# Optimization experiments

Hardware: AMD Instinct MI355X
Metric: run time of the kernel (lower is better)

The kernel has to match this reference:

```python
import jax, jax.numpy as jnp
import numpy as np
import math

EPS = 1e-5      # artanh boundary clamp (Poincare ball)
MIN_NORM = 1e-15

def _norm(x):
    return jnp.clip(jnp.linalg.norm(x, axis=-1, keepdims=True), MIN_NORM, None)

def artanh(x):
    x = jnp.clip(x, -1.0 + EPS, 1.0 - EPS)
    return 0.5 * (jnp.log1p(x) - jnp.log1p(-x))

def expmap0(u):
    # c = 1 Poincare ball: tanh(||u||) * u / ||u||
    n = _norm(u)
    return jnp.tanh(n) * u / n

def mobius_matvec(M, x):
    # geoopt: mx = x @ M^T; res = tanh(||mx||/||x|| * artanh(||x||)) * mx/||mx||
    xn = _norm(x)
    mx = x @ M.T
    mxn = _norm(mx)
    res = jnp.tanh(mxn / xn * artanh(xn)) * mx / mxn
    zero_row = jnp.all(mx == 0, axis=-1, keepdims=True)
    return jnp.where(zero_row, jnp.zeros_like(res), res)

def mobius_add(x, y):
    x2 = jnp.sum(x * x, axis=-1, keepdims=True)
    y2 = jnp.sum(y * y, axis=-1, keepdims=True)
    xy = jnp.sum(x * y, axis=-1, keepdims=True)
    num = (1.0 + 2.0 * xy + y2) * x + (1.0 - x2) * y
    den = 1.0 + 2.0 * xy + x2 * y2
    return num / jnp.clip(den, MIN_NORM, None)

def dist(x, y):
    # d(x,y) = 2 * artanh(|| (-x) mobius+ y ||); reduces the last dim
    return 2.0 * artanh(_norm(mobius_add(-x, y)))[..., 0]

def setup_inputs() -> dict:
    key = jax.random.key(0)
    k1, k2, k3, k4, k5 = jax.random.split(key, 5)
    B, S, H, D = 64, 1024, 768, 64
    bound = 1.0 / math.sqrt(D)
    sequence_output = jax.random.normal(k1, (B, S, H), dtype=jnp.float32) * 0.1
    proj = jax.random.uniform(k2, (H, D), dtype=jnp.float32, minval=-0.05, maxval=0.05)
    trans = jax.random.uniform(k3, (D, D), dtype=jnp.float32, minval=-0.05, maxval=0.05)
    pos = expmap0(jax.random.uniform(k4, (D,), dtype=jnp.float32, minval=-bound, maxval=bound))
    neg = expmap0(jax.random.uniform(k5, (D,), dtype=jnp.float32, minval=-bound, maxval=bound))
    return {"sequence_output": sequence_output, "proj": proj, "trans": trans,
            "pos": pos, "neg": neg}

def reference(sequence_output, proj, trans, pos, neg):
    t = sequence_output @ proj          # [B, S, 64]
    t = expmap0(t)
    t = mobius_matvec(trans, t)
    pos_logits = dist(neg, t).sum(-1)   # [B]
    neg_logits = dist(pos, t).sum(-1)   # [B]
    return jnp.stack((neg_logits, pos_logits), axis=-1)  # [B, 2]
```

## Files before the change

### kernel.cpp

```cpp
#include <hip/hip_runtime.h>
#include <math.h>

#define MIN_NORM 1e-15f
#define BOUND_EPS 1e-5f

typedef __attribute__((ext_vector_type(8))) short short8v;
typedef __attribute__((ext_vector_type(4))) float f32x4;

__device__ __forceinline__ unsigned short f2bf(float f) {
  unsigned int u = __float_as_uint(f);
  unsigned int r = (u + 0x7FFFu + ((u >> 16) & 1u)) >> 16;
  return (unsigned short)r;
}

__device__ __forceinline__ float gred16(float v) {
  v += __shfl_xor(v, 1, 64);
  v += __shfl_xor(v, 2, 64);
  v += __shfl_xor(v, 4, 64);
  v += __shfl_xor(v, 8, 64);
  return v;
}
__device__ __forceinline__ float wred64(float v) {
#pragma unroll
  for (int off = 32; off; off >>= 1) v += __shfl_xor(v, off, 64);
  return v;
}
__device__ __forceinline__ float artanh_c(float x) {
  x = fminf(fmaxf(x, -1.f + BOUND_EPS), 1.f - BOUND_EPS);
  return 0.5f * logf((1.f + x) / (1.f - x));
}

__global__ __launch_bounds__(256) void poincare_prep(
    const float* __restrict__ proj, const float* __restrict__ trans,
    unsigned short* __restrict__ projB, unsigned short* __restrict__ transB) {
  int idx = blockIdx.x * 256 + threadIdx.x;
  if (idx < 49152) {
    int j = idx & 7, l = (idx >> 3) & 63, nt = (idx >> 9) & 3, kt = idx >> 11;
    projB[idx] = f2bf(proj[(kt * 32 + (l >> 4) * 8 + j) * 64 + nt * 16 + (l & 15)]);
  } else if (idx < 49152 + 4096) {
    int i2 = idx - 49152;
    int j = i2 & 7, l = (i2 >> 3) & 63, nt = (i2 >> 9) & 3, kt = i2 >> 11;
    transB[i2] = f2bf(trans[(nt * 16 + (l & 15)) * 64 + kt * 32 + (l >> 4) * 8 + j]);
  }
}

__global__ __launch_bounds__(256, 4) void poincare_main(
    const float* __restrict__ seq,
    const unsigned short* __restrict__ projB,
    const unsigned short* __restrict__ transB,
    const float* __restrict__ pos, const float* __restrict__ neg,
    float* __restrict__ wsPart) {
  __shared__ unsigned short teL[4][16 * 64];
  __shared__ float partial[4][2];

  const int tid = threadIdx.x;
  const int w = tid >> 6, l = tid & 63;
  const int lr = l & 15, lk = l >> 4;
  const long bIdx = blockIdx.x;

  const float* pA = seq + ((bIdx * 64 + w * 16 + lr) * 768 + lk * 8);
  const unsigned short* pB = projB + l * 8;

  f32x4 acc[4];
#pragma unroll
  for (int nt = 0; nt < 4; ++nt) acc[nt] = (f32x4){0.f, 0.f, 0.f, 0.f};

  for (int kt = 0; kt < 24; ++kt) {
    float4 a0 = *(const float4*)(pA);
    float4 a1 = *(const float4*)(pA + 4);
    pA += 32;
    const unsigned short* pb = pB + kt * 2048;
    short8v b0 = *(const short8v*)(pb);
    short8v b1 = *(const short8v*)(pb + 512);
    short8v b2 = *(const short8v*)(pb + 1024);
    short8v b3 = *(const short8v*)(pb + 1536);
    short8v av;
    av[0] = (short)f2bf(a0.x); av[1] = (short)f2bf(a0.y);
    av[2] = (short)f2bf(a0.z); av[3] = (short)f2bf(a0.w);
    av[4] = (short)f2bf(a1.x); av[5] = (short)f2bf(a1.y);
    av[6] = (short)f2bf(a1.z); av[7] = (short)f2bf(a1.w);
    acc[0] = __builtin_amdgcn_mfma_f32_16x16x32_bf16(av, b0, acc[0], 0, 0, 0);
    acc[1] = __builtin_amdgcn_mfma_f32_16x16x32_bf16(av, b1, acc[1], 0, 0, 0);
    acc[2] = __builtin_amdgcn_mfma_f32_16x16x32_bf16(av, b2, acc[2], 0, 0, 0);
    acc[3] = __builtin_amdgcn_mfma_f32_16x16x32_bf16(av, b3, acc[3], 0, 0, 0);
  }

  float th[4];
#pragma unroll
  for (int i = 0; i < 4; ++i) {
    float s = acc[0][i] * acc[0][i] + acc[1][i] * acc[1][i] +
              acc[2][i] * acc[2][i] + acc[3][i] * acc[3][i];
    s = gred16(s);
    float n = fmaxf(sqrtf(s), MIN_NORM);
    float t = tanhf(n);
    th[i] = fmaxf(t, MIN_NORM);
    float sc = t / n;
#pragma unroll
    for (int nt = 0; nt < 4; ++nt) acc[nt][i] *= sc;
  }

  unsigned short* buf = teL[w];
#pragma unroll
  for (int i = 0; i < 4; ++i) {
    int row = lk * 4 + i;
    int sw = (row & 7) << 3;
#pragma unroll
    for (int nt = 0; nt < 4; ++nt) {
      int col = nt * 16 + lr;
      buf[row * 64 + (col ^ sw)] = f2bf(acc[nt][i]);
    }
  }
  __syncthreads();

  f32x4 acc2[4];
#pragma unroll
  for (int nt = 0; nt < 4; ++nt) acc2[nt] = (f32x4){0.f, 0.f, 0.f, 0.f};
  const unsigned short* pT = transB + l * 8;
#pragma unroll
  for (int kt = 0; kt < 2; ++kt) {
    short8v a2 = *(const short8v*)&buf[lr * 64 + ((kt * 32 + lk * 8) ^ ((lr & 7) << 3))];
    const unsigned short* pt = pT + kt * 2048;
    short8v c0 = *(const short8v*)(pt);
    short8v c1 = *(const short8v*)(pt + 512);
    short8v c2 = *(const short8v*)(pt + 1024);
    short8v c3 = *(const short8v*)(pt + 1536);
    acc2[0] = __builtin_amdgcn_mfma_f32_16x16x32_bf16(a2, c0, acc2[0], 0, 0, 0);
    acc2[1] = __builtin_amdgcn_mfma_f32_16x16x32_bf16(a2, c1, acc2[1], 0, 0, 0);
    acc2[2] = __builtin_amdgcn_mfma_f32_16x16x32_bf16(a2, c2, acc2[2], 0, 0, 0);
    acc2[3] = __builtin_amdgcn_mfma_f32_16x16x32_bf16(a2, c3, acc2[3], 0, 0, 0);
  }

  float xp[4], xq[4];
#pragma unroll
  for (int nt = 0; nt < 4; ++nt) {
    xp[nt] = pos[nt * 16 + lr];
    xq[nt] = neg[nt * 16 + lr];
  }
  float x2p = wred64(xp[0] * xp[0] + xp[1] * xp[1] + xp[2] * xp[2] + xp[3] * xp[3]) * 0.25f;
  float x2n = wred64(xq[0] * xq[0] + xq[1] * xq[1] + xq[2] * xq[2] + xq[3] * xq[3]) * 0.25f;

  float distP = 0.f, distN = 0.f;
#pragma unroll
  for (int i = 0; i < 4; ++i) {
    float m0 = acc2[0][i], m1 = acc2[1][i], m2 = acc2[2][i], m3 = acc2[3][i];
    float s = gred16(m0 * m0 + m1 * m1 + m2 * m2 + m3 * m3);
    float mxn = fmaxf(sqrtf(s), MIN_NORM);
    float xn = th[i];
    float rs = tanhf(mxn / xn * artanh_c(xn)) / mxn;
    float r0 = rs * m0, r1 = rs * m1, r2 = rs * m2, r3 = rs * m3;
    float y2 = gred16(r0 * r0 + r1 * r1 + r2 * r2 + r3 * r3);
    float xyP = -gred16(xp[0] * r0 + xp[1] * r1 + xp[2] * r2 + xp[3] * r3);
    float xyN = -gred16(xq[0] * r0 + xq[1] * r1 + xq[2] * r2 + xq[3] * r3);
    {
      float A = 1.f + 2.f * xyP + y2, B = 1.f - x2p;
      float inv = 1.f / fmaxf(1.f + 2.f * xyP + x2p * y2, MIN_NORM);
      float v0 = (B * r0 - A * xp[0]) * inv, v1 = (B * r1 - A * xp[1]) * inv;
      float v2 = (B * r2 - A * xp[2]) * inv, v3 = (B * r3 - A * xp[3]) * inv;
      float nv = fmaxf(sqrtf(gred16(v0 * v0 + v1 * v1 + v2 * v2 + v3 * v3)), MIN_NORM);
      distP += 2.f * artanh_c(nv);
    }
    {
      float A = 1.f + 2.f * xyN + y2, B = 1.f - x2n;
      float inv = 1.f / fmaxf(1.f + 2.f * xyN + x2n * y2, MIN_NORM);
      float v0 = (B * r0 - A * xq[0]) * inv, v1 = (B * r1 - A * xq[1]) * inv;
      float v2 = (B * r2 - A * xq[2]) * inv, v3 = (B * r3 - A * xq[3]) * inv;
      float nv = fmaxf(sqrtf(gred16(v0 * v0 + v1 * v1 + v2 * v2 + v3 * v3)), MIN_NORM);
      distN += 2.f * artanh_c(nv);
    }
  }
  float tP = wred64(distP) * 0.0625f;
  float tN = wred64(distN) * 0.0625f;
  if (l == 0) { partial[w][0] = tP; partial[w][1] = tN; }
  __syncthreads();
  if (tid == 0)
    wsPart[bIdx * 2 + 0] = partial[0][0] + partial[1][0] + partial[2][0] + partial[3][0];
  if (tid == 1)
    wsPart[bIdx * 2 + 1] = partial[0][1] + partial[1][1] + partial[2][1] + partial[3][1];
}

__global__ __launch_bounds__(128) void poincare_reduce(const float* __restrict__ wsPart,
                                                       float* __restrict__ out) {
  int t = threadIdx.x;
  int b = t >> 1, j = t & 1;
  float s = 0.f;
#pragma unroll
  for (int i = 0; i < 16; ++i) s += wsPart[(b * 16 + i) * 2 + j];
  out[b * 2 + j] = s;
}

extern "C" void kernel_launch(void* const* d_in, const int* in_sizes, int n_in,
                              void* d_out, int out_size, void* d_ws, size_t ws_size,
                              hipStream_t stream) {
  const float* seq = (const float*)d_in[0];
  const float* proj = (const float*)d_in[1];
  const float* trans = (const float*)d_in[2];
  const float* pos = (const float*)d_in[3];
  const float* neg = (const float*)d_in[4];

  unsigned short* projB = (unsigned short*)d_ws;
  unsigned short* transB = projB + 49152;
  float* wsPart = (float*)((char*)d_ws + 106496);
  float* out = (float*)d_out;

  poincare_prep<<<208, 256, 0, stream>>>(proj, trans, projB, transB);
  poincare_main<<<1024, 256, 0, stream>>>(seq, projB, transB, pos, neg, wsPart);
  poincare_reduce<<<1, 128, 0, stream>>>(wsPart, out);
}
```

Before: 54.81 us.

## Split GEMM K dimension across two wave groups with LDS reduction

The main kernel now uses 512 threads per block. Two sets of four waves each compute half of the 768-wide K reduction for the same 64 rows, and the second half's partial accumulators are summed through a padded shared-memory buffer. The aim is to double the number of waves in flight, so the memory-bound streaming of the sequence input hides latency better. The cost is extra LDS traffic, two more barriers, and half the waves sitting idle during the epilogue.

```diff
diff --git a/kernel.cpp b/kernel.cpp
--- a/kernel.cpp
+++ b/kernel.cpp
@@ -44,28 +44,30 @@
   }
 }
 
-__global__ __launch_bounds__(256, 4) void poincare_main(
+__global__ __launch_bounds__(512, 8) void poincare_main(
     const float* __restrict__ seq,
     const unsigned short* __restrict__ projB,
     const unsigned short* __restrict__ transB,
     const float* __restrict__ pos, const float* __restrict__ neg,
     float* __restrict__ wsPart) {
   __shared__ unsigned short teL[4][16 * 64];
+  __shared__ float xbuf[4][64][17];
   __shared__ float partial[4][2];
 
   const int tid = threadIdx.x;
   const int w = tid >> 6, l = tid & 63;
+  const int p = w & 3, h = w >> 2;
   const int lr = l & 15, lk = l >> 4;
   const long bIdx = blockIdx.x;
 
-  const float* pA = seq + ((bIdx * 64 + w * 16 + lr) * 768 + lk * 8);
-  const unsigned short* pB = projB + l * 8;
+  const float* pA = seq + ((bIdx * 64 + p * 16 + lr) * 768 + h * 384 + lk * 8);
+  const unsigned short* pB = projB + h * 12 * 2048 + l * 8;
 
   f32x4 acc[4];
 #pragma unroll
   for (int nt = 0; nt < 4; ++nt) acc[nt] = (f32x4){0.f, 0.f, 0.f, 0.f};
 
-  for (int kt = 0; kt < 24; ++kt) {
+  for (int kt = 0; kt < 12; ++kt) {
     float4 a0 = *(const float4*)(pA);
     float4 a1 = *(const float4*)(pA + 4);
     pA += 32;
@@ -85,97 +87,115 @@
     acc[3] = __builtin_amdgcn_mfma_f32_16x16x32_bf16(av, b3, acc[3], 0, 0, 0);
   }
 
+  if (h) {
+#pragma unroll
+    for (int nt = 0; nt < 4; ++nt)
+#pragma unroll
+      for (int i = 0; i < 4; ++i) xbuf[p][l][nt * 4 + i] = acc[nt][i];
+  }
+  __syncthreads();
+
   float th[4];
-#pragma unroll
-  for (int i = 0; i < 4; ++i) {
-    float s = acc[0][i] * acc[0][i] + acc[1][i] * acc[1][i] +
-              acc[2][i] * acc[2][i] + acc[3][i] * acc[3][i];
-    s = gred16(s);
-    float n = fmaxf(sqrtf(s), MIN_NORM);
-    float t = tanhf(n);
-    th[i] = fmaxf(t, MIN_NORM);
-    float sc = t / n;
-#pragma unroll
-    for (int nt = 0; nt < 4; ++nt) acc[nt][i] *= sc;
-  }
-
-  unsigned short* buf = teL[w];
-#pragma unroll
-  for (int i = 0; i < 4; ++i) {
-    int row = lk * 4 + i;
-    int sw = (row & 7) << 3;
+  if (!h) {
+#pragma unroll
+    for (int nt = 0; nt < 4; ++nt)
+#pragma unroll
+      for (int i = 0; i < 4; ++i) acc[nt][i] += xbuf[p][l][nt * 4 + i];
+
+#pragma unroll
+    for (int i = 0; i < 4; ++i) {
+      float s = acc[0][i] * acc[0][i] + acc[1][i] * acc[1][i] +
+                acc[2][i] * acc[2][i] + acc[3][i] * acc[3][i];
+      s = gred16(s);
+      float n = fmaxf(sqrtf(s), MIN_NORM);
+      float t = tanhf(n);
+      th[i] = fmaxf(t, MIN_NORM);
+      float sc = t / n;
+#pragma unroll
+      for (int nt = 0; nt < 4; ++nt) acc[nt][i] *= sc;
+    }
+
+    unsigned short* buf = teL[p];
+#pragma unroll
+    for (int i = 0; i < 4; ++i) {
+      int row = lk * 4 + i;
+      int sw = (row & 7) << 3;
+#pragma unroll
+      for (int nt = 0; nt < 4; ++nt) {
+        int col = nt * 16 + lr;
+        buf[row * 64 + (col ^ sw)] = f2bf(acc[nt][i]);
+      }
+    }
+  }
+  __syncthreads();
+
+  if (!h) {
+    const unsigned short* buf = teL[p];
+    f32x4 acc2[4];
+#pragma unroll
+    for (int nt = 0; nt < 4; ++nt) acc2[nt] = (f32x4){0.f, 0.f, 0.f, 0.f};
+    const unsigned short* pT = transB + l * 8;
+#pragma unroll
+    for (int kt = 0; kt < 2; ++kt) {
+      short8v a2 = *(const short8v*)&buf[lr * 64 + ((kt * 32 + lk * 8) ^ ((lr & 7) << 3))];
+      const unsigned short* pt = pT + kt * 2048;
+      short8v c0 = *(const short8v*)(pt);
+      short8v c1 = *(const short8v*)(pt + 512);
+      short8v c2 = *(const short8v*)(pt + 1024);
+      short8v c3 = *(const short8v*)(pt + 1536);
+      acc2[0] = __builtin_amdgcn_mfma_f32_16x16x32_bf16(a2, c0, acc2[0], 0, 0, 0);
+      acc2[1] = __builtin_amdgcn_mfma_f32_16x16x32_bf16(a2, c1, acc2[1], 0, 0, 0);
+      acc2[2] = __builtin_amdgcn_mfma_f32_16x16x32_bf16(a2, c2, acc2[2], 0, 0, 0);
+      acc2[3] = __builtin_amdgcn_mfma_f32_16x16x32_bf16(a2, c3, acc2[3], 0, 0, 0);
+    }
+
+    float xp[4], xq[4];
 #pragma unroll
     for (int nt = 0; nt < 4; ++nt) {
-      int col = nt * 16 + lr;
-      buf[row * 64 + (col ^ sw)] = f2bf(acc[nt][i]);
-    }
+      xp[nt] = pos[nt * 16 + lr];
+      xq[nt] = neg[nt * 16 + lr];
+    }
+    float x2p = wred64(xp[0] * xp[0] + xp[1] * xp[1] + xp[2] * xp[2] + xp[3] * xp[3]) * 0.25f;
+    float x2n = wred64(xq[0] * xq[0] + xq[1] * xq[1] + xq[2] * xq[2] + xq[3] * xq[3]) * 0.25f;
+
+    float distP = 0.f, distN = 0.f;
+#pragma unroll
+    for (int i = 0; i < 4; ++i) {
+      float m0 = acc2[0][i], m1 = acc2[1][i], m2 = acc2[2][i], m3 = acc2[3][i];
+      float s = gred16(m0 * m0 + m1 * m1 + m2 * m2 + m3 * m3);
+      float mxn = fmaxf(sqrtf(s), MIN_NORM);
+      float xn = th[i];
+      float rs = tanhf(mxn / xn * artanh_c(xn)) / mxn;
+      float r0 = rs * m0, r1 = rs * m1, r2 = rs * m2, r3 = rs * m3;
+      float y2 = gred16(r0 * r0 + r1 * r1 + r2 * r2 + r3 * r3);
+      float xyP = -gred16(xp[0] * r0 + xp[1] * r1 + xp[2] * r2 + xp[3] * r3);
+      float xyN = -gred16(xq[0] * r0 + xq[1] * r1 + xq[2] * r2 + xq[3] * r3);
+      {
+        float A = 1.f + 2.f * xyP + y2, B = 1.f - x2p;
+        float inv = 1.f / fmaxf(1.f + 2.f * xyP + x2p * y2, MIN_NORM);
+        float v0 = (B * r0 - A * xp[0]) * inv, v1 = (B * r1 - A * xp[1]) * inv;
+        float v2 = (B * r2 - A * xp[2]) * inv, v3 = (B * r3 - A * xp[3]) * inv;
+        float nv = fmaxf(sqrtf(gred16(v0 * v0 + v1 * v1 + v2 * v2 + v3 * v3)), MIN_NORM);
+        distP += 2.f * artanh_c(nv);
+      }
+      {
+        float A = 1.f + 2.f * xyN + y2, B = 1.f - x2n;
+        float inv = 1.f / fmaxf(1.f + 2.f * xyN + x2n * y2, MIN_NORM);
+        float v0 = (B * r0 - A * xq[0]) * inv, v1 = (B * r1 - A * xq[1]) * inv;
+        float v2 = (B * r2 - A * xq[2]) * inv, v3 = (B * r3 - A * xq[3]) * inv;
+        float nv = fmaxf(sqrtf(gred16(v0 * v0 + v1 * v1 + v2 * v2 + v3 * v3)), MIN_NORM);
+        distN += 2.f * artanh_c(nv);
+      }
+    }
+    float tP = wred64(distP) * 0.0625f;
+    float tN = wred64(distN) * 0.0625f;
+    if (l == 0) { partial[p][0] = tP; partial[p][1] = tN; }
   }
   __syncthreads();
-
-  f32x4 acc2[4];
-#pragma unroll
-  for (int nt = 0; nt < 4; ++nt) acc2[nt] = (f32x4){0.f, 0.f, 0.f, 0.f};
-  const unsigned short* pT = transB + l * 8;
-#pragma unroll
-  for (int kt = 0; kt < 2; ++kt) {
-    short8v a2 = *(const short8v*)&buf[lr * 64 + ((kt * 32 + lk * 8) ^ ((lr & 7) << 3))];
-    const unsigned short* pt = pT + kt * 2048;
-    short8v c0 = *(const short8v*)(pt);
-    short8v c1 = *(const short8v*)(pt + 512);
-    short8v c2 = *(const short8v*)(pt + 1024);
-    short8v c3 = *(const short8v*)(pt + 1536);
-    acc2[0] = __builtin_amdgcn_mfma_f32_16x16x32_bf16(a2, c0, acc2[0], 0, 0, 0);
-    acc2[1] = __builtin_amdgcn_mfma_f32_16x16x32_bf16(a2, c1, acc2[1], 0, 0, 0);
-    acc2[2] = __builtin_amdgcn_mfma_f32_16x16x32_bf16(a2, c2, acc2[2], 0, 0, 0);
-    acc2[3] = __builtin_amdgcn_mfma_f32_16x16x32_bf16(a2, c3, acc2[3], 0, 0, 0);
-  }
-
-  float xp[4], xq[4];
-#pragma unroll
-  for (int nt = 0; nt < 4; ++nt) {
-    xp[nt] = pos[nt * 16 + lr];
-    xq[nt] = neg[nt * 16 + lr];
-  }
-  float x2p = wred64(xp[0] * xp[0] + xp[1] * xp[1] + xp[2] * xp[2] + xp[3] * xp[3]) * 0.25f;
-  float x2n = wred64(xq[0] * xq[0] + xq[1] * xq[1] + xq[2] * xq[2] + xq[3] * xq[3]) * 0.25f;
-
-  float distP = 0.f, distN = 0.f;
-#pragma unroll
-  for (int i = 0; i < 4; ++i) {
-    float m0 = acc2[0][i], m1 = acc2[1][i], m2 = acc2[2][i], m3 = acc2[3][i];
-    float s = gred16(m0 * m0 + m1 * m1 + m2 * m2 + m3 * m3);
-    float mxn = fmaxf(sqrtf(s), MIN_NORM);
-    float xn = th[i];
-    float rs = tanhf(mxn / xn * artanh_c(xn)) / mxn;
-    float r0 = rs * m0, r1 = rs * m1, r2 = rs * m2, r3 = rs * m3;
-    float y2 = gred16(r0 * r0 + r1 * r1 + r2 * r2 + r3 * r3);
-    float xyP = -gred16(xp[0] * r0 + xp[1] * r1 + xp[2] * r2 + xp[3] * r3);
-    float xyN = -gred16(xq[0] * r0 + xq[1] * r1 + xq[2] * r2 + xq[3] * r3);
-    {
-      float A = 1.f + 2.f * xyP + y2, B = 1.f - x2p;
-      float inv = 1.f / fmaxf(1.f + 2.f * xyP + x2p * y2, MIN_NORM);
-      float v0 = (B * r0 - A * xp[0]) * inv, v1 = (B * r1 - A * xp[1]) * inv;
-      float v2 = (B * r2 - A * xp[2]) * inv, v3 = (B * r3 - A * xp[3]) * inv;
-      float nv = fmaxf(sqrtf(gred16(v0 * v0 + v1 * v1 + v2 * v2 + v3 * v3)), MIN_NORM);
-      distP += 2.f * artanh_c(nv);
-    }
-    {
-      float A = 1.f + 2.f * xyN + y2, B = 1.f - x2n;
-      float inv = 1.f / fmaxf(1.f + 2.f * xyN + x2n * y2, MIN_NORM);
-      float v0 = (B * r0 - A * xq[0]) * inv, v1 = (B * r1 - A * xq[1]) * inv;
-      float v2 = (B * r2 - A * xq[2]) * inv, v3 = (B * r3 - A * xq[3]) * inv;
-      float nv = fmaxf(sqrtf(gred16(v0 * v0 + v1 * v1 + v2 * v2 + v3 * v3)), MIN_NORM);
-      distN += 2.f * artanh_c(nv);
-    }
-  }
-  float tP = wred64(distP) * 0.0625f;
-  float tN = wred64(distN) * 0.0625f;
-  if (l == 0) { partial[w][0] = tP; partial[w][1] = tN; }
-  __syncthreads();
-  if (tid == 0)
+  if (tid == 0) {
     wsPart[bIdx * 2 + 0] = partial[0][0] + partial[1][0] + partial[2][0] + partial[3][0];
-  if (tid == 1)
     wsPart[bIdx * 2 + 1] = partial[0][1] + partial[1][1] + partial[2][1] + partial[3][1];
+  }
 }
 
 __global__ __launch_bounds__(128) void poincare_reduce(const float* __restrict__ wsPart,
@@ -203,6 +223,6 @@
   float* out = (float*)d_out;
 
   poincare_prep<<<208, 256, 0, stream>>>(proj, trans, projB, transB);
-  poincare_main<<<1024, 256, 0, stream>>>(seq, projB, transB, pos, neg, wsPart);
+  poincare_main<<<1024, 512, 0, stream>>>(seq, projB, transB, pos, neg, wsPart);
   poincare_reduce<<<1, 128, 0, stream>>>(wsPart, out);
 }
```

After: 53.59 us. 2.2% less time.
